# Optimization experiments

Measured on AMD Instinct MI355X. Metric: run time of the kernel, lower is better.

The kernel has to match this reference:

```python
import jax, jax.numpy as jnp
import numpy as np

B = 16384      # batch
FEAT = 4096    # features
D = 64         # nearest_root_factors(4096) -> (64, 64)
BN_EPS = 1e-3


def setup_inputs() -> dict:
    key = jax.random.key(0)
    ks = jax.random.split(key, 9)
    stdv1 = 1.0 / np.sqrt(D)   # layer1: zero_initialization=False path
    stdv2 = 0.001              # layer2: zero_initialization=True path

    def u(k, shape, s):
        return jax.random.uniform(k, shape, minval=-s, maxval=s, dtype=jnp.float32)

    return {
        "inputs": jax.random.normal(ks[0], (B, FEAT), dtype=jnp.float32),
        "bn0_gamma": jnp.ones((FEAT,), jnp.float32),
        "bn0_beta": jnp.zeros((FEAT,), jnp.float32),
        "bn1_gamma": jnp.ones((FEAT,), jnp.float32),
        "bn1_beta": jnp.zeros((FEAT,), jnp.float32),
        # Kronecker layer 1 (left: weights (o2=input_dim1, o1=out_dim1); right: (d,d))
        "k1_lw": u(ks[1], (D, D), stdv1),
        "k1_lb": u(ks[2], (D, D), stdv1),
        "k1_rw": u(ks[3], (D, D), stdv1),
        "k1_rb": u(ks[4], (D, D), stdv1),
        # Kronecker layer 2 (zero-initialized)
        "k2_lw": u(ks[5], (D, D), stdv2),
        "k2_lb": u(ks[6], (D, D), stdv2),
        "k2_rw": u(ks[7], (D, D), stdv2),
        "k2_rb": u(ks[8], (D, D), stdv2),
    }


def _batch_norm(x, gamma, beta):
    # training-mode BN: biased batch statistics over the batch dim, eps=1e-3
    m = jnp.mean(x, axis=0)
    v = jnp.var(x, axis=0)
    return (x - m) * jax.lax.rsqrt(v + BN_EPS) * gamma + beta


def _kron_block(t, lw, lb, rw, rb):
    # KDLeftLayer: permute(matmul(permute(x,[0,2,1]), W),[0,2,1]) + b
    #   out[b,o,j] = sum_k x[b,k,j] * W[k,o]
    t = jnp.einsum("bkj,ko->boj", t, lw) + lb
    # KDRightLayer: x @ W + b
    t = jnp.matmul(t, rw) + rb
    return t


def reference(inputs, bn0_gamma, bn0_beta, bn1_gamma, bn1_beta,
              k1_lw, k1_lb, k1_rw, k1_rb, k2_lw, k2_lb, k2_rw, k2_rb):
    t = jax.nn.relu(_batch_norm(inputs, bn0_gamma, bn0_beta))
    t = t.reshape(-1, D, D)
    t = _kron_block(t, k1_lw, k1_lb, k1_rw, k1_rb).reshape(-1, FEAT)
    t = jax.nn.relu(_batch_norm(t, bn1_gamma, bn1_beta))
    # dropout p=0.0 -> identity
    t = t.reshape(-1, D, D)
    t = _kron_block(t, k2_lw, k2_lb, k2_rw, k2_rb).reshape(-1, FEAT)
    return inputs + t
```

## Files before the change

kernel.cpp:

```cpp
#include <hip/hip_runtime.h>

#define NROWS 16384
#define NFEAT 4096

typedef __attribute__((ext_vector_type(8))) short          bfrag8;
typedef __attribute__((ext_vector_type(4))) float          fvec4;
typedef __attribute__((ext_vector_type(2))) float          fvec2;
typedef __attribute__((ext_vector_type(4))) unsigned short usvec4;
typedef __attribute__((ext_vector_type(8))) unsigned short usvec8;
typedef __attribute__((ext_vector_type(2))) unsigned int   uvec2;
typedef __attribute__((ext_vector_type(4))) unsigned int   uvec4;

#define WS_P0   ((size_t)0)
#define WS_P1   ((size_t)16 << 20)
#define WS_SC0  ((size_t)48 << 20)
#define WS_SH0  (WS_SC0 + 16384)
#define WS_SC1  (WS_SC0 + 32768)
#define WS_SH1  (WS_SC0 + 49152)
#define WS_C1   (WS_SC0 + 65536)
#define WS_C2   (WS_SC0 + 81920)
#define WS_T1   ((size_t)64 << 20)
#define WS_XB   ((size_t)192 << 20)

__device__ __forceinline__ unsigned short f2bf_bits(float f) {
  unsigned u = __builtin_bit_cast(unsigned, f);
  u += 0x7FFFu + ((u >> 16) & 1u);
  return (unsigned short)(u >> 16);
}
__device__ __forceinline__ float bf2f(unsigned short b) {
  return __builtin_bit_cast(float, ((unsigned)b) << 16);
}
__device__ __forceinline__ usvec4 pack4(fvec4 a) {
  usvec4 p;
#pragma unroll
  for (int e = 0; e < 4; ++e) p[e] = f2bf_bits(a[e]);
  return p;
}
__device__ __forceinline__ fvec4 unpack4(usvec4 p) {
  return fvec4{bf2f(p[0]), bf2f(p[1]), bf2f(p[2]), bf2f(p[3])};
}
__device__ __forceinline__ int swz64(int i) { return i ^ (((i >> 6) & 7) << 2); }
__device__ __forceinline__ int swz32(int i) { return i ^ (((i >> 5) & 7) << 2); }

__global__ __launch_bounds__(256) void k_bn0part(const float* __restrict__ x,
                                                 unsigned short* __restrict__ p0,
                                                 unsigned short* __restrict__ xb) {
  const int t = threadIdx.x, p = blockIdx.x;
  fvec4 s[4], sq[4];
#pragma unroll
  for (int q = 0; q < 4; ++q) { s[q] = fvec4{0.f,0.f,0.f,0.f}; sq[q] = s[q]; }
  for (int r = p * 16; r < p * 16 + 16; ++r) {
    const fvec4* row = (const fvec4*)(x + (size_t)r * NFEAT);
    usvec4* xrow = (usvec4*)(xb + (size_t)r * NFEAT);
#pragma unroll
    for (int q = 0; q < 4; ++q) {
      fvec4 v = row[t + 256 * q];
      s[q] += v; sq[q] += v * v;
      xrow[t + 256 * q] = pack4(v);
    }
  }
#pragma unroll
  for (int q = 0; q < 4; ++q) {
    int f0 = (t + 256 * q) * 4;
    *(usvec4*)(p0 + (size_t)p * 8192 + f0)        = pack4(s[q]);
    *(usvec4*)(p0 + (size_t)p * 8192 + 4096 + f0) = pack4(sq[q]);
  }
}

__device__ __forceinline__ void red_body(fvec4 (*red)[16][2],
                                         const unsigned short* __restrict__ parts,
                                         int nsets,
                                         const float* __restrict__ g,
                                         const float* __restrict__ bta,
                                         float* __restrict__ sc_out,
                                         float* __restrict__ sh_out, int j) {
  const int t = threadIdx.x;
  const int fc = t & 15, c = t >> 4;
  const int v = j * 64 + fc * 4;
  fvec4 s = fvec4{0.f,0.f,0.f,0.f}, q = s;
  for (int i = c; i < nsets; i += 16) {
    s += unpack4(*(const usvec4*)(parts + (size_t)i * 8192 + v));
    q += unpack4(*(const usvec4*)(parts + (size_t)i * 8192 + 4096 + v));
  }
  red[c][fc][0] = s; red[c][fc][1] = q;
  __syncthreads();
  if (c == 0) {
    fvec4 S = red[0][fc][0], Q = red[0][fc][1];
#pragma unroll
    for (int k = 1; k < 16; ++k) { S += red[k][fc][0]; Q += red[k][fc][1]; }
    fvec4 SC, SH;
    const float inv = 1.0f / NROWS;
#pragma unroll
    for (int e = 0; e < 4; ++e) {
      float mean = S[e] * inv;
      float var  = Q[e] * inv - mean * mean;
      float scv  = g[v + e] * rsqrtf(var + 1e-3f);
      SC[e] = scv; SH[e] = bta[v + e] - mean * scv;
    }
    *(fvec4*)(sc_out + v) = SC;
    *(fvec4*)(sh_out + v) = SH;
  }
}

__global__ __launch_bounds__(256) void k_prep0(const unsigned short* __restrict__ p0,
                                               const float* __restrict__ g0,
                                               const float* __restrict__ b0,
                                               float* __restrict__ sc0,
                                               float* __restrict__ sh0,
                                               const float* __restrict__ lb1,
                                               const float* __restrict__ rw1,
                                               const float* __restrict__ rb1,
                                               const float* __restrict__ lb2,
                                               const float* __restrict__ rw2,
                                               const float* __restrict__ rb2,
                                               float* __restrict__ c1,
                                               float* __restrict__ c2) {
  __shared__ fvec4 red[16][16][2];
  if (blockIdx.x < 64) {
    red_body(red, p0, 1024, g0, b0, sc0, sh0, blockIdx.x);
  } else {
    const int bb   = blockIdx.x - 64;
    const int idx  = (bb & 15) * 256 + threadIdx.x;
    const int part = bb >> 4;
    const float* lb = part ? lb2 : lb1;
    const float* rw = part ? rw2 : rw1;
    const float* rb = part ? rb2 : rb1;
    int r = idx >> 6, o = idx & 63;
    float acc = rb[o * 64 + r];
    for (int j = 0; j < 64; ++j) acc += lb[o * 64 + j] * rw[j * 64 + r];
    (part ? c2 : c1)[o * 64 + r] = acc;
  }
}

__global__ __launch_bounds__(256) void k_bn1stat(const unsigned char* __restrict__ t1q,
                                                 unsigned short* __restrict__ p1) {
  const int t = threadIdx.x, p = blockIdx.x;
  float s[16], q[16];
#pragma unroll
  for (int i = 0; i < 16; ++i) { s[i] = 0.f; q[i] = 0.f; }
  for (int r = p * 16; r < p * 16 + 16; ++r) {
    uvec4 v = *(const uvec4*)(t1q + (size_t)r * NFEAT + t * 16);
#pragma unroll
    for (int d = 0; d < 4; ++d) {
      fvec2 lo = __builtin_amdgcn_cvt_pk_f32_fp8((int)v[d], false);
      fvec2 hi = __builtin_amdgcn_cvt_pk_f32_fp8((int)v[d], true);
      float e0 = lo[0], e1 = lo[1], e2 = hi[0], e3 = hi[1];
      s[d*4+0] += e0; q[d*4+0] += e0*e0;
      s[d*4+1] += e1; q[d*4+1] += e1*e1;
      s[d*4+2] += e2; q[d*4+2] += e2*e2;
      s[d*4+3] += e3; q[d*4+3] += e3*e3;
    }
  }
#pragma unroll
  for (int b4 = 0; b4 < 4; ++b4) {
    fvec4 sv{s[b4*4], s[b4*4+1], s[b4*4+2], s[b4*4+3]};
    fvec4 qv{q[b4*4], q[b4*4+1], q[b4*4+2], q[b4*4+3]};
    *(usvec4*)(p1 + (size_t)p * 8192 + t * 16 + b4 * 4)        = pack4(sv);
    *(usvec4*)(p1 + (size_t)p * 8192 + 4096 + t * 16 + b4 * 4) = pack4(qv);
  }
}

__global__ __launch_bounds__(256) void k_red1(const unsigned short* __restrict__ p1,
                                              const float* __restrict__ g1,
                                              const float* __restrict__ b1,
                                              float* __restrict__ sc1,
                                              float* __restrict__ sh1) {
  __shared__ fvec4 red[16][16][2];
  red_body(red, p1, 1024, g1, b1, sc1, sh1, blockIdx.x);
}

template <int LAYER>
__global__ __launch_bounds__(256, 2) void k_kron(const unsigned short* __restrict__ xb,
                                                 const unsigned char* __restrict__ t1r,
                                                 const float* __restrict__ lw,
                                                 const float* __restrict__ rw,
                                                 const float* __restrict__ scv,
                                                 const float* __restrict__ shv,
                                                 const float* __restrict__ cn,
                                                 unsigned char* __restrict__ t1w,
                                                 float* __restrict__ outf) {
  __shared__ __align__(16) unsigned short vt[4][4096];
  __shared__ __align__(16) unsigned scsh[4096];
  __shared__ __align__(16) unsigned cbl[2048];
  const int tid = threadIdx.x, bid = blockIdx.x;
  const int w = tid >> 6, l = tid & 63, m = l & 15, g = l >> 4;
  unsigned short* vtw = &vt[w][0];

#pragma unroll
  for (int c = 0; c < 16; ++c) {
    int f = tid * 16 + c;
    scsh[swz64(f)] = (unsigned)f2bf_bits(scv[f]) | ((unsigned)f2bf_bits(shv[f]) << 16);
  }
#pragma unroll
  for (int c = 0; c < 8; ++c) {
    int d = tid * 8 + c;
    int o = d >> 5, pr = (d & 31) * 2;
    cbl[swz32(d)] = (unsigned)f2bf_bits(cn[o * 64 + pr]) |
                    ((unsigned)f2bf_bits(cn[o * 64 + pr + 1]) << 16);
  }
#pragma unroll
  for (int c = 0; c < 8; ++c)
    *(uvec4*)((char*)vtw + l * 128 + c * 16) = uvec4{0u, 0u, 0u, 0u};

  bfrag8 frw[4][2];
#pragma unroll
  for (int rt = 0; rt < 4; ++rt)
#pragma unroll
    for (int ks = 0; ks < 2; ++ks)
#pragma unroll
      for (int i = 0; i < 8; ++i)
        frw[rt][ks][i] = (short)f2bf_bits(rw[(ks * 32 + g * 8 + i) * 64 + rt * 16 + m]);

  bfrag8 flw[4][2];
#pragma unroll
  for (int ot = 0; ot < 4; ++ot)
#pragma unroll
    for (int ks = 0; ks < 2; ++ks)
#pragma unroll
      for (int i = 0; i < 8; ++i)
        flw[ot][ks][i] = (short)f2bf_bits(lw[(ks * 32 + g * 8 + i) * 64 + ot * 16 + m]);

  __syncthreads();

  const int r0w = bid * 32 + w * 8;

  usvec8 sA0[8], sA1[8];
  uvec2  sQ0[8], sQ1[8];

  if constexpr (LAYER == 1) {
    const usvec8* p = (const usvec8*)(xb + (size_t)r0w * NFEAT);
#pragma unroll
    for (int kt = 0; kt < 4; ++kt)
#pragma unroll
      for (int ks = 0; ks < 2; ++ks)
        sA0[kt * 2 + ks] = p[(kt * 16 + m) * 8 + ks * 4 + g];
  } else {
    const uvec2* p = (const uvec2*)(t1r + (size_t)r0w * NFEAT);
#pragma unroll
    for (int kt = 0; kt < 4; ++kt)
#pragma unroll
      for (int ks = 0; ks < 2; ++ks)
        sQ0[kt * 2 + ks] = p[(kt * 16 + m) * 8 + ks * 4 + g];
  }

  auto row_body = [&](int rrow, usvec8 (&curA)[8], usvec8 (&nxtA)[8],
                      uvec2 (&curQ)[8], uvec2 (&nxtQ)[8], bool pf) {
    if (pf) {
      if constexpr (LAYER == 1) {
        const usvec8* p = (const usvec8*)(xb + (size_t)(rrow + 1) * NFEAT);
#pragma unroll
        for (int kt = 0; kt < 4; ++kt)
#pragma unroll
          for (int ks = 0; ks < 2; ++ks)
            nxtA[kt * 2 + ks] = p[(kt * 16 + m) * 8 + ks * 4 + g];
      } else {
        const uvec2* p = (const uvec2*)(t1r + (size_t)(rrow + 1) * NFEAT);
#pragma unroll
        for (int kt = 0; kt < 4; ++kt)
#pragma unroll
          for (int ks = 0; ks < 2; ++ks)
            nxtQ[kt * 2 + ks] = p[(kt * 16 + m) * 8 + ks * 4 + g];
      }
    }
    usvec4 res[16];
    if constexpr (LAYER == 2) {
#pragma unroll
      for (int ot = 0; ot < 4; ++ot)
#pragma unroll
        for (int rt2 = 0; rt2 < 4; ++rt2)
          res[ot * 4 + rt2] = *(const usvec4*)(xb + (size_t)rrow * NFEAT +
                                               (ot * 16 + m) * 64 + rt2 * 16 + g * 4);
    }

#pragma unroll
    for (int kt = 0; kt < 4; ++kt) {
      bfrag8 fa[2];
#pragma unroll
      for (int ks = 0; ks < 2; ++ks) {
        int f0 = (kt * 16 + m) * 64 + ks * 32 + g * 8;
        uvec4 c0  = *(const uvec4*)&scsh[swz64(f0)];
        uvec4 c1v = *(const uvec4*)&scsh[swz64(f0 + 4)];
        float xs[8];
        if constexpr (LAYER == 1) {
          usvec8 tv = curA[kt * 2 + ks];
#pragma unroll
          for (int i = 0; i < 8; ++i) xs[i] = bf2f(tv[i]);
        } else {
          uvec2 tv = curQ[kt * 2 + ks];
          fvec2 d0 = __builtin_amdgcn_cvt_pk_f32_fp8((int)tv[0], false);
          fvec2 d1 = __builtin_amdgcn_cvt_pk_f32_fp8((int)tv[0], true);
          fvec2 d2 = __builtin_amdgcn_cvt_pk_f32_fp8((int)tv[1], false);
          fvec2 d3 = __builtin_amdgcn_cvt_pk_f32_fp8((int)tv[1], true);
          xs[0]=d0[0]; xs[1]=d0[1]; xs[2]=d1[0]; xs[3]=d1[1];
          xs[4]=d2[0]; xs[5]=d2[1]; xs[6]=d3[0]; xs[7]=d3[1];
        }
        usvec8 u;
#pragma unroll
        for (int i = 0; i < 8; ++i) {
          unsigned dw = (i < 4) ? c0[i] : c1v[i - 4];
          float scf = __builtin_bit_cast(float, dw << 16);
          float shf = __builtin_bit_cast(float, dw & 0xffff0000u);
          u[i] = f2bf_bits(fmaxf(fmaf(xs[i], scf, shf), 0.f));
        }
        fa[ks] = __builtin_bit_cast(bfrag8, u);
      }
#pragma unroll
      for (int rt = 0; rt < 4; ++rt) {
        fvec4 va = fvec4{0.f, 0.f, 0.f, 0.f};
        va = __builtin_amdgcn_mfma_f32_16x16x32_bf16(fa[0], frw[rt][0], va, 0, 0, 0);
        va = __builtin_amdgcn_mfma_f32_16x16x32_bf16(fa[1], frw[rt][1], va, 0, 0, 0);
        int ridx = rt * 16 + m;
        int chunk = 2 * kt + (g >> 1);
        int byte = ridx * 128 + ((chunk ^ (ridx & 7)) << 4) + (g & 1) * 8;
        *(usvec4*)((char*)vtw + byte) = pack4(va);
      }
    }

    __builtin_amdgcn_sched_barrier(0);
    asm volatile("s_waitcnt lgkmcnt(0)");
    __builtin_amdgcn_sched_barrier(0);

#pragma unroll
    for (int rt2 = 0; rt2 < 4; ++rt2) {
      int ridx = rt2 * 16 + m;
      bfrag8 a0 = *(const bfrag8*)((const char*)vtw +
                    ridx * 128 + (((0 + g) ^ (ridx & 7)) << 4));
      bfrag8 a1 = *(const bfrag8*)((const char*)vtw +
                    ridx * 128 + (((4 + g) ^ (ridx & 7)) << 4));
      fvec4 acc[4];
#pragma unroll
      for (int ot = 0; ot < 4; ++ot) {
        acc[ot] = fvec4{0.f, 0.f, 0.f, 0.f};
        acc[ot] = __builtin_amdgcn_mfma_f32_16x16x32_bf16(a0, flw[ot][0], acc[ot], 0, 0, 0);
        acc[ot] = __builtin_amdgcn_mfma_f32_16x16x32_bf16(a1, flw[ot][1], acc[ot], 0, 0, 0);
      }
#pragma unroll
      for (int ot = 0; ot < 4; ++ot) {
        int dcb = (ot * 16 + m) * 32 + rt2 * 8 + 2 * g;
        uvec2 cv = *(const uvec2*)&cbl[swz32(dcb)];
        fvec4 cb4{__builtin_bit_cast(float, cv[0] << 16),
                  __builtin_bit_cast(float, cv[0] & 0xffff0000u),
                  __builtin_bit_cast(float, cv[1] << 16),
                  __builtin_bit_cast(float, cv[1] & 0xffff0000u)};
        fvec4 z = acc[ot] + cb4;
        int foff = (ot * 16 + m) * 64 + rt2 * 16 + g * 4;
        if constexpr (LAYER == 1) {
          int pq = __builtin_amdgcn_cvt_pk_fp8_f32(z[0], z[1], 0, false);
          pq     = __builtin_amdgcn_cvt_pk_fp8_f32(z[2], z[3], pq, true);
          *(unsigned*)(t1w + (size_t)rrow * NFEAT + foff) = (unsigned)pq;
        } else {
          *(fvec4*)(outf + (size_t)rrow * NFEAT + foff) =
              unpack4(res[ot * 4 + rt2]) + z;
        }
      }
    }
  };

  for (int rp = 0; rp < 4; ++rp) {
    row_body(r0w + 2 * rp,     sA0, sA1, sQ0, sQ1, true);
    row_body(r0w + 2 * rp + 1, sA1, sA0, sQ1, sQ0, rp < 3);
  }
}

extern "C" void kernel_launch(void* const* d_in, const int* in_sizes, int n_in,
                              void* d_out, int out_size, void* d_ws, size_t ws_size,
                              hipStream_t stream) {
  (void)in_sizes; (void)n_in; (void)out_size; (void)ws_size;
  const float* x    = (const float*)d_in[0];
  const float* g0   = (const float*)d_in[1];
  const float* b0   = (const float*)d_in[2];
  const float* g1   = (const float*)d_in[3];
  const float* b1   = (const float*)d_in[4];
  const float* k1lw = (const float*)d_in[5];
  const float* k1lb = (const float*)d_in[6];
  const float* k1rw = (const float*)d_in[7];
  const float* k1rb = (const float*)d_in[8];
  const float* k2lw = (const float*)d_in[9];
  const float* k2lb = (const float*)d_in[10];
  const float* k2rw = (const float*)d_in[11];
  const float* k2rb = (const float*)d_in[12];
  char* ws = (char*)d_ws;

  unsigned short* p0  = (unsigned short*)(ws + WS_P0);
  unsigned short* p1  = (unsigned short*)(ws + WS_P1);
  unsigned char*  t1q = (unsigned char*)(ws + WS_T1);
  unsigned short* xb  = (unsigned short*)(ws + WS_XB);
  float* sc0 = (float*)(ws + WS_SC0);
  float* sh0 = (float*)(ws + WS_SH0);
  float* sc1 = (float*)(ws + WS_SC1);
  float* sh1 = (float*)(ws + WS_SH1);
  float* c1  = (float*)(ws + WS_C1);
  float* c2  = (float*)(ws + WS_C2);

  k_bn0part<<<1024, 256, 0, stream>>>(x, p0, xb);
  k_prep0<<<96, 256, 0, stream>>>(p0, g0, b0, sc0, sh0,
                                  k1lb, k1rw, k1rb, k2lb, k2rw, k2rb, c1, c2);
  k_kron<1><<<512, 256, 0, stream>>>(xb, nullptr, k1lw, k1rw, sc0, sh0, c1,
                                     t1q, nullptr);
  k_bn1stat<<<1024, 256, 0, stream>>>(t1q, p1);
  k_red1<<<64, 256, 0, stream>>>(p1, g1, b1, sc1, sh1);
  k_kron<2><<<512, 256, 0, stream>>>(xb, t1q, k2lw, k2rw, sc1, sh1, c2,
                                     t1q, (float*)d_out);
}
```

Measured before the change: 326.1 us.

## Precompute packed bf16 bias in prep, drop LDS bias table, raise kron occupancy

The k_prep0 kernel now writes the combined bias term already packed as bf16 pairs, so the kron kernel reads it straight from global/L2 instead of building an LDS table in every block. The kron kernel frees that LDS, raises launch bounds to 3 blocks per CU, halves the rows per block (1024 blocks instead of 512), and prefetches two rows ahead with a 2-slot register ring instead of one. The aim is more resident waves to hide memory latency and less per-block setup. In exchange, the bias is fetched from global memory on every row, and the tighter register budget could cause spills.

```diff
diff --git a/kernel.cpp b/kernel.cpp
--- a/kernel.cpp
+++ b/kernel.cpp
@@ -17,8 +17,8 @@
 #define WS_SH0  (WS_SC0 + 16384)
 #define WS_SC1  (WS_SC0 + 32768)
 #define WS_SH1  (WS_SC0 + 49152)
-#define WS_C1   (WS_SC0 + 65536)
-#define WS_C2   (WS_SC0 + 81920)
+#define WS_C1P  (WS_SC0 + 65536)
+#define WS_C2P  (WS_SC0 + 81920)
 #define WS_T1   ((size_t)64 << 20)
 #define WS_XB   ((size_t)192 << 20)
 
@@ -40,7 +40,6 @@
   return fvec4{bf2f(p[0]), bf2f(p[1]), bf2f(p[2]), bf2f(p[3])};
 }
 __device__ __forceinline__ int swz64(int i) { return i ^ (((i >> 6) & 7) << 2); }
-__device__ __forceinline__ int swz32(int i) { return i ^ (((i >> 5) & 7) << 2); }
 
 __global__ __launch_bounds__(256) void k_bn0part(const float* __restrict__ x,
                                                  unsigned short* __restrict__ p0,
@@ -113,9 +112,10 @@
                                                const float* __restrict__ lb2,
                                                const float* __restrict__ rw2,
                                                const float* __restrict__ rb2,
-                                               float* __restrict__ c1,
-                                               float* __restrict__ c2) {
+                                               unsigned* __restrict__ c1p,
+                                               unsigned* __restrict__ c2p) {
   __shared__ fvec4 red[16][16][2];
+  __shared__ float shc[256];
   if (blockIdx.x < 64) {
     red_body(red, p0, 1024, g0, b0, sc0, sh0, blockIdx.x);
   } else {
@@ -128,7 +128,13 @@
     int r = idx >> 6, o = idx & 63;
     float acc = rb[o * 64 + r];
     for (int j = 0; j < 64; ++j) acc += lb[o * 64 + j] * rw[j * 64 + r];
-    (part ? c2 : c1)[o * 64 + r] = acc;
+    shc[threadIdx.x] = acc;
+    __syncthreads();
+    if (!(idx & 64)) {
+      float accO = shc[threadIdx.x ^ 64];
+      unsigned pk = (unsigned)f2bf_bits(acc) | ((unsigned)f2bf_bits(accO) << 16);
+      (part ? c2p : c1p)[o * 32 + (r >> 1)] = pk;
+    }
   }
 }
 
@@ -170,18 +176,17 @@
 }
 
 template <int LAYER>
-__global__ __launch_bounds__(256, 2) void k_kron(const unsigned short* __restrict__ xb,
+__global__ __launch_bounds__(256, 3) void k_kron(const unsigned short* __restrict__ xb,
                                                  const unsigned char* __restrict__ t1r,
                                                  const float* __restrict__ lw,
                                                  const float* __restrict__ rw,
                                                  const float* __restrict__ scv,
                                                  const float* __restrict__ shv,
-                                                 const float* __restrict__ cn,
+                                                 const unsigned* __restrict__ cnp,
                                                  unsigned char* __restrict__ t1w,
                                                  float* __restrict__ outf) {
   __shared__ __align__(16) unsigned short vt[4][4096];
   __shared__ __align__(16) unsigned scsh[4096];
-  __shared__ __align__(16) unsigned cbl[2048];
   const int tid = threadIdx.x, bid = blockIdx.x;
   const int w = tid >> 6, l = tid & 63, m = l & 15, g = l >> 4;
   unsigned short* vtw = &vt[w][0];
@@ -192,13 +197,6 @@
     scsh[swz64(f)] = (unsigned)f2bf_bits(scv[f]) | ((unsigned)f2bf_bits(shv[f]) << 16);
   }
 #pragma unroll
-  for (int c = 0; c < 8; ++c) {
-    int d = tid * 8 + c;
-    int o = d >> 5, pr = (d & 31) * 2;
-    cbl[swz32(d)] = (unsigned)f2bf_bits(cn[o * 64 + pr]) |
-                    ((unsigned)f2bf_bits(cn[o * 64 + pr + 1]) << 16);
-  }
-#pragma unroll
   for (int c = 0; c < 8; ++c)
     *(uvec4*)((char*)vtw + l * 128 + c * 16) = uvec4{0u, 0u, 0u, 0u};
 
@@ -222,46 +220,38 @@
 
   __syncthreads();
 
-  const int r0w = bid * 32 + w * 8;
-
-  usvec8 sA0[8], sA1[8];
-  uvec2  sQ0[8], sQ1[8];
+  const int r0w = bid * 16 + w * 4;
+
+  usvec8 sA[2][8];
+  uvec2  sQ[2][8];
 
   if constexpr (LAYER == 1) {
-    const usvec8* p = (const usvec8*)(xb + (size_t)r0w * NFEAT);
+    const usvec8* pr0 = (const usvec8*)(xb + (size_t)r0w * NFEAT);
+    const usvec8* pr1 = (const usvec8*)(xb + (size_t)(r0w + 1) * NFEAT);
 #pragma unroll
     for (int kt = 0; kt < 4; ++kt)
 #pragma unroll
-      for (int ks = 0; ks < 2; ++ks)
-        sA0[kt * 2 + ks] = p[(kt * 16 + m) * 8 + ks * 4 + g];
+      for (int ks = 0; ks < 2; ++ks) {
+        sA[0][kt * 2 + ks] = pr0[(kt * 16 + m) * 8 + ks * 4 + g];
+        sA[1][kt * 2 + ks] = pr1[(kt * 16 + m) * 8 + ks * 4 + g];
+      }
   } else {
-    const uvec2* p = (const uvec2*)(t1r + (size_t)r0w * NFEAT);
+    const uvec2* pr0 = (const uvec2*)(t1r + (size_t)r0w * NFEAT);
+    const uvec2* pr1 = (const uvec2*)(t1r + (size_t)(r0w + 1) * NFEAT);
 #pragma unroll
     for (int kt = 0; kt < 4; ++kt)
 #pragma unroll
-      for (int ks = 0; ks < 2; ++ks)
-        sQ0[kt * 2 + ks] = p[(kt * 16 + m) * 8 + ks * 4 + g];
-  }
-
-  auto row_body = [&](int rrow, usvec8 (&curA)[8], usvec8 (&nxtA)[8],
-                      uvec2 (&curQ)[8], uvec2 (&nxtQ)[8], bool pf) {
-    if (pf) {
-      if constexpr (LAYER == 1) {
-        const usvec8* p = (const usvec8*)(xb + (size_t)(rrow + 1) * NFEAT);
-#pragma unroll
-        for (int kt = 0; kt < 4; ++kt)
-#pragma unroll
-          for (int ks = 0; ks < 2; ++ks)
-            nxtA[kt * 2 + ks] = p[(kt * 16 + m) * 8 + ks * 4 + g];
-      } else {
-        const uvec2* p = (const uvec2*)(t1r + (size_t)(rrow + 1) * NFEAT);
-#pragma unroll
-        for (int kt = 0; kt < 4; ++kt)
-#pragma unroll
-          for (int ks = 0; ks < 2; ++ks)
-            nxtQ[kt * 2 + ks] = p[(kt * 16 + m) * 8 + ks * 4 + g];
-      }
-    }
+      for (int ks = 0; ks < 2; ++ks) {
+        sQ[0][kt * 2 + ks] = pr0[(kt * 16 + m) * 8 + ks * 4 + g];
+        sQ[1][kt * 2 + ks] = pr1[(kt * 16 + m) * 8 + ks * 4 + g];
+      }
+  }
+
+#pragma unroll
+  for (int rr = 0; rr < 4; ++rr) {
+    const int rrow = r0w + rr;
+    const int cur = rr & 1;
+
     usvec4 res[16];
     if constexpr (LAYER == 2) {
 #pragma unroll
@@ -282,11 +272,11 @@
         uvec4 c1v = *(const uvec4*)&scsh[swz64(f0 + 4)];
         float xs[8];
         if constexpr (LAYER == 1) {
-          usvec8 tv = curA[kt * 2 + ks];
+          usvec8 tv = sA[cur][kt * 2 + ks];
 #pragma unroll
           for (int i = 0; i < 8; ++i) xs[i] = bf2f(tv[i]);
         } else {
-          uvec2 tv = curQ[kt * 2 + ks];
+          uvec2 tv = sQ[cur][kt * 2 + ks];
           fvec2 d0 = __builtin_amdgcn_cvt_pk_f32_fp8((int)tv[0], false);
           fvec2 d1 = __builtin_amdgcn_cvt_pk_f32_fp8((int)tv[0], true);
           fvec2 d2 = __builtin_amdgcn_cvt_pk_f32_fp8((int)tv[1], false);
@@ -316,9 +306,34 @@
       }
     }
 
+    if (rr + 2 < 4) {
+      if constexpr (LAYER == 1) {
+        const usvec8* p = (const usvec8*)(xb + (size_t)(rrow + 2) * NFEAT);
+#pragma unroll
+        for (int kt = 0; kt < 4; ++kt)
+#pragma unroll
+          for (int ks = 0; ks < 2; ++ks)
+            sA[cur][kt * 2 + ks] = p[(kt * 16 + m) * 8 + ks * 4 + g];
+      } else {
+        const uvec2* p = (const uvec2*)(t1r + (size_t)(rrow + 2) * NFEAT);
+#pragma unroll
+        for (int kt = 0; kt < 4; ++kt)
+#pragma unroll
+          for (int ks = 0; ks < 2; ++ks)
+            sQ[cur][kt * 2 + ks] = p[(kt * 16 + m) * 8 + ks * 4 + g];
+      }
+    }
+
     __builtin_amdgcn_sched_barrier(0);
     asm volatile("s_waitcnt lgkmcnt(0)");
     __builtin_amdgcn_sched_barrier(0);
+
+    uvec2 cbv[16];
+#pragma unroll
+    for (int rt2 = 0; rt2 < 4; ++rt2)
+#pragma unroll
+      for (int ot = 0; ot < 4; ++ot)
+        cbv[rt2 * 4 + ot] = *(const uvec2*)(cnp + (ot * 16 + m) * 32 + rt2 * 8 + g * 2);
 
 #pragma unroll
     for (int rt2 = 0; rt2 < 4; ++rt2) {
@@ -336,8 +351,7 @@
       }
 #pragma unroll
       for (int ot = 0; ot < 4; ++ot) {
-        int dcb = (ot * 16 + m) * 32 + rt2 * 8 + 2 * g;
-        uvec2 cv = *(const uvec2*)&cbl[swz32(dcb)];
+        uvec2 cv = cbv[rt2 * 4 + ot];
         fvec4 cb4{__builtin_bit_cast(float, cv[0] << 16),
                   __builtin_bit_cast(float, cv[0] & 0xffff0000u),
                   __builtin_bit_cast(float, cv[1] << 16),
@@ -354,11 +368,6 @@
         }
       }
     }
-  };
-
-  for (int rp = 0; rp < 4; ++rp) {
-    row_body(r0w + 2 * rp,     sA0, sA1, sQ0, sQ1, true);
-    row_body(r0w + 2 * rp + 1, sA1, sA0, sQ1, sQ0, rp < 3);
   }
 }
 
@@ -389,16 +398,16 @@
   float* sh0 = (float*)(ws + WS_SH0);
   float* sc1 = (float*)(ws + WS_SC1);
   float* sh1 = (float*)(ws + WS_SH1);
-  float* c1  = (float*)(ws + WS_C1);
-  float* c2  = (float*)(ws + WS_C2);
+  unsigned* c1p = (unsigned*)(ws + WS_C1P);
+  unsigned* c2p = (unsigned*)(ws + WS_C2P);
 
   k_bn0part<<<1024, 256, 0, stream>>>(x, p0, xb);
   k_prep0<<<96, 256, 0, stream>>>(p0, g0, b0, sc0, sh0,
-                                  k1lb, k1rw, k1rb, k2lb, k2rw, k2rb, c1, c2);
-  k_kron<1><<<512, 256, 0, stream>>>(xb, nullptr, k1lw, k1rw, sc0, sh0, c1,
-                                     t1q, nullptr);
+                                  k1lb, k1rw, k1rb, k2lb, k2rw, k2rb, c1p, c2p);
+  k_kron<1><<<1024, 256, 0, stream>>>(xb, nullptr, k1lw, k1rw, sc0, sh0, c1p,
+                                      t1q, nullptr);
   k_bn1stat<<<1024, 256, 0, stream>>>(t1q, p1);
   k_red1<<<64, 256, 0, stream>>>(p1, g1, b1, sc1, sh1);
-  k_kron<2><<<512, 256, 0, stream>>>(xb, t1q, k2lw, k2rw, sc1, sh1, c2,
-                                     t1q, (float*)d_out);
-}
+  k_kron<2><<<1024, 256, 0, stream>>>(xb, t1q, k2lw, k2rw, sc1, sh1, c2p,
+                                      t1q, (float*)d_out);
+}
```

After: 598.5 us. 1.84x slower.
